# Kernel optimization log

Measured on AMD Instinct MI355X. Metric: run time of the kernel, lower is better.

Reference implementation:

```python
import jax, jax.numpy as jnp
import numpy as np

COUNT = 8  # hardcoded 8x8 patch grid in the original module


def setup_inputs() -> dict:
    key = jax.random.key(0)
    kx, = jax.random.split(key, 1)
    x = jax.random.normal(kx, (8, 64, 512, 512), dtype=jnp.float32)
    gamma = jnp.zeros((1,), dtype=jnp.float32)  # nn.Parameter(torch.zeros(1))
    return {"x": x, "gamma": gamma}


def reference(x, gamma):
    B, C, H, W = x.shape
    s = H // COUNT  # stride; original uses height-derived stride for both dims
    # Extract the 8x8 grid of patches without loops:
    # (B,C,H,W) -> (B,C,cnt,s,cnt,s) -> (B,cnt,cnt,C,s,s) -> (B,P,C,s*s)
    p = x.reshape(B, C, COUNT, s, COUNT, s)
    p = p.transpose(0, 2, 4, 1, 3, 5).reshape(B, COUNT * COUNT, C, s * s)
    # channel-channel energy per patch: [B,P,C,C]
    energy = jnp.einsum('bpci,bpdi->bpcd', p, p)
    # DANet trick: max - energy, then softmax over last dim
    energy_new = jnp.max(energy, axis=-1, keepdims=True) - energy
    attention = jax.nn.softmax(energy_new, axis=-1)
    out = jnp.einsum('bpcd,bpdi->bpci', attention, p)
    # reassemble spatial map
    out = out.reshape(B, COUNT, COUNT, C, s, s)
    out = out.transpose(0, 3, 1, 4, 2, 5).reshape(B, C, H, W)
    # NOTE: in the torch code y = x is an alias and x is overwritten in-place,
    # so the final result is gamma * attended + attended.
    return gamma[0] * out + out
```

## Files before the change

kernel.cpp:

```cpp
#include <hip/hip_runtime.h>


#define NW  512
#define HWs 262144
#define NS1 16
#define NS3 16

typedef __attribute__((ext_vector_type(8)))  __bf16 bf8;
typedef __attribute__((ext_vector_type(4)))  __bf16 bf4;
typedef __attribute__((ext_vector_type(16))) float  f32x16;

#define F4C(v, k) ((k) == 0 ? (v).x : (k) == 1 ? (v).y : (k) == 2 ? (v).z : (v).w)

__device__ __forceinline__ void bar_lgkm() {
  asm volatile("s_waitcnt lgkmcnt(0)" ::: "memory");
  __builtin_amdgcn_s_barrier();
}

__device__ __forceinline__ void load1(const float* g1, int st, float4 (&R)[16]) {
  const float* gp = g1 + (size_t)st * 4 * NW;
#pragma unroll
  for (int rl = 0; rl < 4; ++rl)
#pragma unroll
    for (int j = 0; j < 4; ++j)
      R[rl * 4 + j] = *(const float4*)(gp + (size_t)rl * NW + j * 4);
}

__device__ __forceinline__ void cvtw1(char* wH, char* wL, int q_ld, int swzw,
                                      const float4 (&R)[16]) {
#pragma unroll
  for (int rl = 0; rl < 4; ++rl)
#pragma unroll
    for (int s = 0; s < 2; ++s) {
      const float4 va = R[rl * 4 + s * 2], vb = R[rl * 4 + s * 2 + 1];
      const float f[8] = {va.x, va.y, va.z, va.w, vb.x, vb.y, vb.z, vb.w};
      bf8 h, lo;
#pragma unroll
      for (int e = 0; e < 8; ++e) {
        h[e]  = (__bf16)f[e];
        lo[e] = (__bf16)(f[e] - (float)h[e]);
      }
      const int boff = (rl * 128 + q_ld * 32 + s * 16) ^ swzw;
      *(bf8*)(wH + boff) = h;
      *(bf8*)(wL + boff) = lo;
    }
}

__device__ __forceinline__ void load3(const float* g3, int st, float4 (&R)[16]) {
  const float* gp = g3 + (size_t)st * 4 * NW;
#pragma unroll
  for (int cc = 0; cc < 4; ++cc)
#pragma unroll
    for (int j = 0; j < 4; ++j)
      R[cc * 4 + j] = *(const float4*)(gp + (size_t)cc * HWs + j * 4);
}

__device__ __forceinline__ void cvtw3(char* sT, int cg, int iq, const float4 (&R)[16]) {
#pragma unroll
  for (int w = 0; w < 16; ++w) {
    bf4 q;
#pragma unroll
    for (int cc = 0; cc < 4; ++cc)
      q[cc] = (__bf16)F4C(R[cc * 4 + (w >> 2)], w & 3);
    const int iloc = iq * 16 + w;
    const int sw   = ((iloc & 15) ^ ((iloc >> 4) & 7)) << 4;
    const int boff = (iloc & 127) * 256 + ((((iloc >> 7) << 7) + cg * 8) ^ sw);
    *(bf4*)(sT + boff) = q;
  }
}

extern "C" __global__ __launch_bounds__(256, 2)
void spectralAgg_kernel(const float* __restrict__ x, const float* __restrict__ g,
                        float* __restrict__ out) {
  __shared__ char lds[73728];
  char* sH = lds;
  char* sL = lds + 32768;
  char* sA = lds + 65536;

  const int t   = threadIdx.x;
  const int wv  = t >> 6;
  const int l   = t & 63;
  const int l31 = l & 31;
  const int hh  = l >> 5;

  const int wg = blockIdx.x;
  const int b  = wg >> 6;
  const int pp = wg & 63;
  const int pr = pp >> 3, pc = pp & 7;
  const size_t pbase = (size_t)b * 64 * HWs + (size_t)(pr * 64) * NW + (size_t)(pc * 64);
  const float* xp = x + pbase;
  float* op = out + pbase;

  const int c_ld = t >> 2, q_ld = t & 3;
  const float* g1 = xp + (size_t)c_ld * HWs + q_ld * 16;
  char* wH = sH + c_ld * 512;
  char* wL = sL + c_ld * 512;
  const int swzw = (c_ld & 31) << 4;

  const int ct = wv >> 1, dt = wv & 1;
  const char* pA  = sH + (size_t)(ct * 32 + l31) * 512;
  const char* pBh = sH + (size_t)(dt * 32 + l31) * 512;
  const char* pBl = sL + (size_t)(dt * 32 + l31) * 512;
  const int swzr = l31 << 4;

  f32x16 accG, accS;
#pragma unroll
  for (int r = 0; r < 16; ++r) { accG[r] = 0.f; accS[r] = 0.f; }

  float4 ra[16], rb[16];
  load1(g1, 0, ra);

  for (int st = 0; st < NS1; ++st) {
    load1(g1, (st + 1 < NS1) ? st + 1 : st, rb);
    cvtw1(wH, wL, q_ld, swzw, ra);
    bar_lgkm();
#pragma unroll
    for (int k0 = 0; k0 < 16; ++k0) {
      const int off = (k0 * 32 + hh * 16) ^ swzr;
      const bf8 a  = *(const bf8*)(pA  + off);
      const bf8 bh = *(const bf8*)(pBh + off);
      const bf8 bl = *(const bf8*)(pBl + off);
      accG = __builtin_amdgcn_mfma_f32_32x32x16_bf16(a, bh, accG, 0, 0, 0);
      accS = __builtin_amdgcn_mfma_f32_32x32x16_bf16(a, bl, accS, 0, 0, 0);
    }
    bar_lgkm();
#pragma unroll
    for (int e = 0; e < 16; ++e) ra[e] = rb[e];
  }

  float* S_lds = (float*)sL;
  float* E_lds = (float*)sH;
#pragma unroll
  for (int r = 0; r < 16; ++r) {
    const int cr = ct * 32 + (r & 3) + ((r >> 2) << 3) + (hh << 2);
    S_lds[cr * 64 + dt * 32 + l31] = accS[r];
  }
  bar_lgkm();
#pragma unroll
  for (int r = 0; r < 16; ++r) {
    const int cr = ct * 32 + (r & 3) + ((r >> 2) << 3) + (hh << 2);
    const int d  = dt * 32 + l31;
    E_lds[cr * 64 + d] = accG[r] + accS[r] + S_lds[d * 64 + cr];
  }
  bar_lgkm();

  const int cg = t >> 4, iq = t & 15;
  const float* g3 = xp + (size_t)(cg * 4) * HWs + (size_t)(iq >> 2) * NW + (iq & 3) * 16;
  load3(g3, 0, ra);

  const float gs = 1.0f + g[0];
#pragma unroll 1
  for (int rr = 0; rr < 16; ++rr) {
    const int c = wv * 16 + rr;
    const float e = E_lds[c * 64 + l];
    float mn = e;
#pragma unroll
    for (int o = 32; o; o >>= 1) mn = fminf(mn, __shfl_xor(mn, o));
    const float w = __expf(mn - e);
    float s = w;
#pragma unroll
    for (int o = 32; o; o >>= 1) s += __shfl_xor(s, o);
    const float a = gs * w / s;
    *(__bf16*)(sA + c * 128 + ((l * 2) ^ ((c & 7) << 4))) = (__bf16)a;
  }
  bar_lgkm();

  bf8 bfr[2][4];
#pragma unroll
  for (int c2 = 0; c2 < 2; ++c2)
#pragma unroll
    for (int k0 = 0; k0 < 4; ++k0)
      bfr[c2][k0] = *(const bf8*)(sA + (size_t)(c2 * 32 + l31) * 128 +
                                  ((k0 * 32 + hh * 16) ^ ((l31 & 7) << 4)));

  for (int st = 0; st < NS3; ++st) {
    load3(g3, (st + 1 < NS3) ? st + 1 : st, rb);
    cvtw3(sH, cg, iq, ra);
    bar_lgkm();

    f32x16 oo[2][2];
#pragma unroll
    for (int it = 0; it < 2; ++it)
#pragma unroll
      for (int c2 = 0; c2 < 2; ++c2)
#pragma unroll
        for (int r = 0; r < 16; ++r) oo[it][c2][r] = 0.f;

#pragma unroll
    for (int it = 0; it < 2; ++it) {
      const int i = wv * 64 + it * 32 + l31;
      const char* base = sH + (size_t)(i & 127) * 256;
      const int hb = (i >> 7) * 128;
      const int sw = ((i & 15) ^ ((i >> 4) & 7)) << 4;
#pragma unroll
      for (int k0 = 0; k0 < 4; ++k0) {
        const bf8 pa = *(const bf8*)(base + ((hb + k0 * 32 + hh * 16) ^ sw));
        oo[it][0] = __builtin_amdgcn_mfma_f32_32x32x16_bf16(pa, bfr[0][k0], oo[it][0], 0, 0, 0);
        oo[it][1] = __builtin_amdgcn_mfma_f32_32x32x16_bf16(pa, bfr[1][k0], oo[it][1], 0, 0, 0);
      }
    }

#pragma unroll
    for (int it = 0; it < 2; ++it)
#pragma unroll
      for (int c2 = 0; c2 < 2; ++c2) {
        const size_t cof = (size_t)(c2 * 32 + l31) * HWs;
#pragma unroll
        for (int rq = 0; rq < 4; ++rq) {
          const int iloc = wv * 64 + it * 32 + rq * 8 + hh * 4;
          const int grow = st * 4 + (iloc >> 6), gcol = iloc & 63;
          float4 q;
          q.x = oo[it][c2][rq * 4 + 0];
          q.y = oo[it][c2][rq * 4 + 1];
          q.z = oo[it][c2][rq * 4 + 2];
          q.w = oo[it][c2][rq * 4 + 3];
          *(float4*)(op + cof + (size_t)grow * NW + gcol) = q;
        }
      }
    bar_lgkm();
#pragma unroll
    for (int e = 0; e < 16; ++e) ra[e] = rb[e];
  }
}

extern "C" void kernel_launch(void* const* d_in, const int* in_sizes, int n_in,
                              void* d_out, int out_size, void* d_ws, size_t ws_size,
                              hipStream_t stream) {
  const float* x = (const float*)d_in[0];
  const float* g = (const float*)d_in[1];
  float* o = (float*)d_out;
  spectralAgg_kernel<<<dim3(512), dim3(256), 0, stream>>>(x, g, o);
}
```

Before: 378.0 us.

## Double block to 512 threads with split-K Gram and halved register staging

Raises the workgroup to 512 threads (8 waves). The Gram phase now splits the K dimension across two wave halves and reduces their partial results through LDS, and each thread stages fewer fp32 loads (8 float4 instead of 32). The second phase re-lays out the transposed patch tile with a padded 144-byte row stride, and LDS shrinks to 64KB so more waves can be resident. The aim is more latency hiding and less register pressure, at the cost of extra LDS reduction passes and barriers.

New measurement: 387.9 us. 2.6% more time.

```diff
diff --git a/kernel.cpp b/kernel.cpp
--- a/kernel.cpp
+++ b/kernel.cpp
@@ -1,122 +1,82 @@
 #include <hip/hip_runtime.h>
 
 
-#define NW  512
-#define HWs 262144
-#define NS1 16
-#define NS3 16
+#define NW   512
+#define HWs  262144
+#define NS   16
 
 typedef __attribute__((ext_vector_type(8)))  __bf16 bf8;
 typedef __attribute__((ext_vector_type(4)))  __bf16 bf4;
 typedef __attribute__((ext_vector_type(16))) float  f32x16;
 
-#define F4C(v, k) ((k) == 0 ? (v).x : (k) == 1 ? (v).y : (k) == 2 ? (v).z : (v).w)
+#define F4E(v,j) ((j)==0?(v).x:(j)==1?(v).y:(j)==2?(v).z:(v).w)
 
 __device__ __forceinline__ void bar_lgkm() {
   asm volatile("s_waitcnt lgkmcnt(0)" ::: "memory");
   __builtin_amdgcn_s_barrier();
 }
 
-__device__ __forceinline__ void load1(const float* g1, int st, float4 (&R)[16]) {
-  const float* gp = g1 + (size_t)st * 4 * NW;
-#pragma unroll
-  for (int rl = 0; rl < 4; ++rl)
-#pragma unroll
-    for (int j = 0; j < 4; ++j)
-      R[rl * 4 + j] = *(const float4*)(gp + (size_t)rl * NW + j * 4);
-}
-
-__device__ __forceinline__ void cvtw1(char* wH, char* wL, int q_ld, int swzw,
-                                      const float4 (&R)[16]) {
-#pragma unroll
-  for (int rl = 0; rl < 4; ++rl)
-#pragma unroll
-    for (int s = 0; s < 2; ++s) {
-      const float4 va = R[rl * 4 + s * 2], vb = R[rl * 4 + s * 2 + 1];
-      const float f[8] = {va.x, va.y, va.z, va.w, vb.x, vb.y, vb.z, vb.w};
-      bf8 h, lo;
-#pragma unroll
-      for (int e = 0; e < 8; ++e) {
-        h[e]  = (__bf16)f[e];
-        lo[e] = (__bf16)(f[e] - (float)h[e]);
-      }
-      const int boff = (rl * 128 + q_ld * 32 + s * 16) ^ swzw;
-      *(bf8*)(wH + boff) = h;
-      *(bf8*)(wL + boff) = lo;
-    }
-}
-
-__device__ __forceinline__ void load3(const float* g3, int st, float4 (&R)[16]) {
-  const float* gp = g3 + (size_t)st * 4 * NW;
-#pragma unroll
-  for (int cc = 0; cc < 4; ++cc)
-#pragma unroll
-    for (int j = 0; j < 4; ++j)
-      R[cc * 4 + j] = *(const float4*)(gp + (size_t)cc * HWs + j * 4);
-}
-
-__device__ __forceinline__ void cvtw3(char* sT, int cg, int iq, const float4 (&R)[16]) {
-#pragma unroll
-  for (int w = 0; w < 16; ++w) {
-    bf4 q;
-#pragma unroll
-    for (int cc = 0; cc < 4; ++cc)
-      q[cc] = (__bf16)F4C(R[cc * 4 + (w >> 2)], w & 3);
-    const int iloc = iq * 16 + w;
-    const int sw   = ((iloc & 15) ^ ((iloc >> 4) & 7)) << 4;
-    const int boff = (iloc & 127) * 256 + ((((iloc >> 7) << 7) + cg * 8) ^ sw);
-    *(bf4*)(sT + boff) = q;
-  }
-}
-
-extern "C" __global__ __launch_bounds__(256, 2)
+extern "C" __global__ __launch_bounds__(512, 4)
 void spectralAgg_kernel(const float* __restrict__ x, const float* __restrict__ g,
                         float* __restrict__ out) {
-  __shared__ char lds[73728];
+  __shared__ char lds[65536];
   char* sH = lds;
   char* sL = lds + 32768;
-  char* sA = lds + 65536;
-
-  const int t   = threadIdx.x;
-  const int wv  = t >> 6;
-  const int l   = t & 63;
+  char* sA = lds + 49152;
+
+  const int T   = threadIdx.x;
+  const int wv8 = T >> 6;
+  const int l   = T & 63;
   const int l31 = l & 31;
   const int hh  = l >> 5;
+  const int g2  = (T >> 4) & 3;
+  const int e16 = T & 15;
 
   const int wg = blockIdx.x;
   const int b  = wg >> 6;
   const int pp = wg & 63;
-  const int pr = pp >> 3, pc = pp & 7;
-  const size_t pbase = (size_t)b * 64 * HWs + (size_t)(pr * 64) * NW + (size_t)(pc * 64);
+  const size_t pbase = (size_t)b*64*HWs + (size_t)((pp>>3)*64)*NW + (size_t)((pp&7)*64);
   const float* xp = x + pbase;
   float* op = out + pbase;
 
-  const int c_ld = t >> 2, q_ld = t & 3;
-  const float* g1 = xp + (size_t)c_ld * HWs + q_ld * 16;
-  char* wH = sH + c_ld * 512;
-  char* wL = sL + c_ld * 512;
-  const int swzw = (c_ld & 31) << 4;
-
-  const int ct = wv >> 1, dt = wv & 1;
-  const char* pA  = sH + (size_t)(ct * 32 + l31) * 512;
-  const char* pBh = sH + (size_t)(dt * 32 + l31) * 512;
-  const char* pBl = sL + (size_t)(dt * 32 + l31) * 512;
-  const int swzr = l31 << 4;
+  float4 ra[8];
+#pragma unroll
+  for (int k = 0; k < 8; ++k)
+    ra[k] = *(const float4*)(xp + (size_t)(k*8+wv8)*HWs + (size_t)g2*NW + e16*4);
+
+  const int q  = wv8 & 3;
+  const int kh = wv8 >> 2;
+  const int ct = q >> 1, dt = q & 1;
+  const char* pA  = sH + (size_t)(ct*32+l31)*512 + kh*256;
+  const char* pBh = sH + (size_t)(dt*32+l31)*512 + kh*256;
+  const char* pBl = sL + (size_t)(dt*32+l31)*512 + kh*256;
+  const int swz1 = (l31 & 15) << 4;
 
   f32x16 accG, accS;
 #pragma unroll
   for (int r = 0; r < 16; ++r) { accG[r] = 0.f; accS[r] = 0.f; }
 
-  float4 ra[16], rb[16];
-  load1(g1, 0, ra);
-
-  for (int st = 0; st < NS1; ++st) {
-    load1(g1, (st + 1 < NS1) ? st + 1 : st, rb);
-    cvtw1(wH, wL, q_ld, swzw, ra);
-    bar_lgkm();
-#pragma unroll
-    for (int k0 = 0; k0 < 16; ++k0) {
-      const int off = (k0 * 32 + hh * 16) ^ swzr;
+  for (int st = 0; st < NS; ++st) {
+#pragma unroll
+    for (int k = 0; k < 8; ++k) {
+      const int c = k*8 + wv8;
+      const float4 v = ra[k];
+      bf4 h, lo;
+      h[0]=(__bf16)v.x; h[1]=(__bf16)v.y; h[2]=(__bf16)v.z; h[3]=(__bf16)v.w;
+      lo[0]=(__bf16)(v.x-(float)h[0]); lo[1]=(__bf16)(v.y-(float)h[1]);
+      lo[2]=(__bf16)(v.z-(float)h[2]); lo[3]=(__bf16)(v.w-(float)h[3]);
+      const int off = c*512 + ((g2*128 + e16*8) ^ ((c&15)<<4));
+      *(bf4*)(sH+off) = h;
+      *(bf4*)(sL+off) = lo;
+    }
+    const int sn = (st+1 < NS) ? st+1 : st;
+#pragma unroll
+    for (int k = 0; k < 8; ++k)
+      ra[k] = *(const float4*)(xp + (size_t)(k*8+wv8)*HWs + (size_t)(sn*4+g2)*NW + e16*4);
+    bar_lgkm();
+#pragma unroll
+    for (int k0 = 0; k0 < 8; ++k0) {
+      const int off = (k0*32 + hh*16) ^ swz1;
       const bf8 a  = *(const bf8*)(pA  + off);
       const bf8 bh = *(const bf8*)(pBh + off);
       const bf8 bl = *(const bf8*)(pBl + off);
@@ -124,35 +84,50 @@
       accS = __builtin_amdgcn_mfma_f32_32x32x16_bf16(a, bl, accS, 0, 0, 0);
     }
     bar_lgkm();
-#pragma unroll
-    for (int e = 0; e < 16; ++e) ra[e] = rb[e];
-  }
-
+  }
+
+  float* E_lds = (float*)sH;
   float* S_lds = (float*)sL;
-  float* E_lds = (float*)sH;
-#pragma unroll
-  for (int r = 0; r < 16; ++r) {
-    const int cr = ct * 32 + (r & 3) + ((r >> 2) << 3) + (hh << 2);
-    S_lds[cr * 64 + dt * 32 + l31] = accS[r];
-  }
-  bar_lgkm();
-#pragma unroll
-  for (int r = 0; r < 16; ++r) {
-    const int cr = ct * 32 + (r & 3) + ((r >> 2) << 3) + (hh << 2);
-    const int d  = dt * 32 + l31;
-    E_lds[cr * 64 + d] = accG[r] + accS[r] + S_lds[d * 64 + cr];
-  }
-  bar_lgkm();
-
-  const int cg = t >> 4, iq = t & 15;
-  const float* g3 = xp + (size_t)(cg * 4) * HWs + (size_t)(iq >> 2) * NW + (iq & 3) * 16;
-  load3(g3, 0, ra);
+  if (kh == 0) {
+#pragma unroll
+    for (int r = 0; r < 16; ++r) {
+      const int cr = ct*32 + (r&3) + ((r>>2)<<3) + (hh<<2);
+      const int d  = dt*32 + l31;
+      S_lds[cr*64+d] = accS[r];
+      E_lds[cr*64+d] = accG[r] + accS[r];
+    }
+  }
+  bar_lgkm();
+  if (kh == 1) {
+#pragma unroll
+    for (int r = 0; r < 16; ++r) {
+      const int cr = ct*32 + (r&3) + ((r>>2)<<3) + (hh<<2);
+      const int d  = dt*32 + l31;
+      S_lds[cr*64+d] += accS[r];
+      E_lds[cr*64+d] += accG[r] + accS[r];
+    }
+  }
+  bar_lgkm();
+#pragma unroll
+  for (int r = 0; r < 8; ++r) {
+    const int c = T >> 3, d = (T&7)*8 + r;
+    E_lds[c*64+d] += S_lds[d*64+c];
+  }
+  bar_lgkm();
+
+  const int quad = (wv8*4+g2) & 15;
+  const int rwb  = (wv8*4+g2) >> 4;
+#pragma unroll
+  for (int k = 0; k < 8; ++k) {
+    const int cc = k & 3, mm = k >> 2;
+    ra[k] = *(const float4*)(xp + (size_t)(quad*4+cc)*HWs + (size_t)(rwb+mm*2)*NW + e16*4);
+  }
 
   const float gs = 1.0f + g[0];
 #pragma unroll 1
-  for (int rr = 0; rr < 16; ++rr) {
-    const int c = wv * 16 + rr;
-    const float e = E_lds[c * 64 + l];
+  for (int rr = 0; rr < 8; ++rr) {
+    const int c = wv8*8 + rr;
+    const float e = E_lds[c*64 + l];
     float mn = e;
 #pragma unroll
     for (int o = 32; o; o >>= 1) mn = fminf(mn, __shfl_xor(mn, o));
@@ -161,65 +136,63 @@
 #pragma unroll
     for (int o = 32; o; o >>= 1) s += __shfl_xor(s, o);
     const float a = gs * w / s;
-    *(__bf16*)(sA + c * 128 + ((l * 2) ^ ((c & 7) << 4))) = (__bf16)a;
-  }
-  bar_lgkm();
-
-  bf8 bfr[2][4];
-#pragma unroll
-  for (int c2 = 0; c2 < 2; ++c2)
-#pragma unroll
-    for (int k0 = 0; k0 < 4; ++k0)
-      bfr[c2][k0] = *(const bf8*)(sA + (size_t)(c2 * 32 + l31) * 128 +
-                                  ((k0 * 32 + hh * 16) ^ ((l31 & 7) << 4)));
-
-  for (int st = 0; st < NS3; ++st) {
-    load3(g3, (st + 1 < NS3) ? st + 1 : st, rb);
-    cvtw3(sH, cg, iq, ra);
-    bar_lgkm();
-
-    f32x16 oo[2][2];
-#pragma unroll
-    for (int it = 0; it < 2; ++it)
-#pragma unroll
-      for (int c2 = 0; c2 < 2; ++c2)
-#pragma unroll
-        for (int r = 0; r < 16; ++r) oo[it][c2][r] = 0.f;
-
-#pragma unroll
-    for (int it = 0; it < 2; ++it) {
-      const int i = wv * 64 + it * 32 + l31;
-      const char* base = sH + (size_t)(i & 127) * 256;
-      const int hb = (i >> 7) * 128;
-      const int sw = ((i & 15) ^ ((i >> 4) & 7)) << 4;
-#pragma unroll
-      for (int k0 = 0; k0 < 4; ++k0) {
-        const bf8 pa = *(const bf8*)(base + ((hb + k0 * 32 + hh * 16) ^ sw));
-        oo[it][0] = __builtin_amdgcn_mfma_f32_32x32x16_bf16(pa, bfr[0][k0], oo[it][0], 0, 0, 0);
-        oo[it][1] = __builtin_amdgcn_mfma_f32_32x32x16_bf16(pa, bfr[1][k0], oo[it][1], 0, 0, 0);
+    *(__bf16*)(sA + c*256 + ((l*2) ^ ((c&15)<<4))) = (__bf16)a;
+  }
+  bar_lgkm();
+
+  char* sT = sH;
+  const char* pP = sT + (size_t)(wv8*32 + l31)*144;
+
+  for (int st = 0; st < NS; ++st) {
+#pragma unroll
+    for (int mm = 0; mm < 2; ++mm) {
+      const int row = rwb + mm*2;
+#pragma unroll
+      for (int jj = 0; jj < 4; ++jj) {
+        const int i = row*64 + e16*4 + jj;
+        bf4 qv;
+        qv[0] = (__bf16)F4E(ra[mm*4+0], jj);
+        qv[1] = (__bf16)F4E(ra[mm*4+1], jj);
+        qv[2] = (__bf16)F4E(ra[mm*4+2], jj);
+        qv[3] = (__bf16)F4E(ra[mm*4+3], jj);
+        *(bf4*)(sT + i*144 + quad*8) = qv;
       }
     }
-
-#pragma unroll
-    for (int it = 0; it < 2; ++it)
-#pragma unroll
-      for (int c2 = 0; c2 < 2; ++c2) {
-        const size_t cof = (size_t)(c2 * 32 + l31) * HWs;
-#pragma unroll
-        for (int rq = 0; rq < 4; ++rq) {
-          const int iloc = wv * 64 + it * 32 + rq * 8 + hh * 4;
-          const int grow = st * 4 + (iloc >> 6), gcol = iloc & 63;
-          float4 q;
-          q.x = oo[it][c2][rq * 4 + 0];
-          q.y = oo[it][c2][rq * 4 + 1];
-          q.z = oo[it][c2][rq * 4 + 2];
-          q.w = oo[it][c2][rq * 4 + 3];
-          *(float4*)(op + cof + (size_t)grow * NW + gcol) = q;
-        }
-      }
-    bar_lgkm();
-#pragma unroll
-    for (int e = 0; e < 16; ++e) ra[e] = rb[e];
+    const int sn = (st+1 < NS) ? st+1 : st;
+#pragma unroll
+    for (int k = 0; k < 8; ++k) {
+      const int cc = k & 3, mm = k >> 2;
+      ra[k] = *(const float4*)(xp + (size_t)(quad*4+cc)*HWs + (size_t)(sn*4+rwb+mm*2)*NW + e16*4);
+    }
+    bar_lgkm();
+
+    f32x16 oo0, oo1;
+#pragma unroll
+    for (int r = 0; r < 16; ++r) { oo0[r] = 0.f; oo1[r] = 0.f; }
+#pragma unroll
+    for (int k0 = 0; k0 < 4; ++k0) {
+      const int sAoff = (k0*32 + hh*16) ^ ((l31&15)<<4);
+      const bf8 pa = *(const bf8*)(pP + k0*32 + hh*16);
+      const bf8 b0 = *(const bf8*)(sA + (size_t)l31*256 + sAoff);
+      const bf8 b1 = *(const bf8*)(sA + (size_t)(32+l31)*256 + sAoff);
+      oo0 = __builtin_amdgcn_mfma_f32_32x32x16_bf16(pa, b0, oo0, 0, 0, 0);
+      oo1 = __builtin_amdgcn_mfma_f32_32x32x16_bf16(pa, b1, oo1, 0, 0, 0);
+    }
+
+#pragma unroll
+    for (int rq = 0; rq < 4; ++rq) {
+      const int iloc = wv8*32 + rq*8 + hh*4;
+      const int gi = st*256 + iloc;
+      const int grow = gi >> 6, gcol = gi & 63;
+      float* oprow = op + (size_t)grow*NW + gcol;
+      float4 q0; q0.x = oo0[rq*4+0]; q0.y = oo0[rq*4+1];
+                 q0.z = oo0[rq*4+2]; q0.w = oo0[rq*4+3];
+      *(float4*)(oprow + (size_t)l31*HWs) = q0;
+      float4 q1; q1.x = oo1[rq*4+0]; q1.y = oo1[rq*4+1];
+                 q1.z = oo1[rq*4+2]; q1.w = oo1[rq*4+3];
+      *(float4*)(oprow + (size_t)(32+l31)*HWs) = q1;
+    }
+    bar_lgkm();
   }
 }
 
@@ -229,5 +202,5 @@
   const float* x = (const float*)d_in[0];
   const float* g = (const float*)d_in[1];
   float* o = (float*)d_out;
-  spectralAgg_kernel<<<dim3(512), dim3(256), 0, stream>>>(x, g, o);
+  spectralAgg_kernel<<<dim3(512), dim3(512), 0, stream>>>(x, g, o);
 }
```

## Split into gram, softmax, and PV kernels with row-strip coalesced loads

Applied to the files above, without the earlier changes.

Replaces the single per-patch kernel with three kernels. In the first and third, each block covers a 16-row strip across all eight patches of a patch row, so global loads and stores run along full 512-wide rows instead of 64-wide patch segments. The first kernel writes partial Gram matrices to workspace, a small kernel sums them and applies the softmax, and the third kernel transposes x in LDS before doing the attention-times-values MFMA. This costs a second read of x, extra workspace traffic and two more launches, and it falls back to the old kernel when the workspace is too small.

New measurement: 412.5 us. 1.09x slower.

```diff
diff --git a/kernel.cpp b/kernel.cpp
--- a/kernel.cpp
+++ b/kernel.cpp
@@ -3,21 +3,245 @@
 
 #define NW  512
 #define HWs 262144
-#define NS1 16
-#define NS3 16
-
+
+typedef __attribute__((ext_vector_type(4)))  __bf16 bf4;
 typedef __attribute__((ext_vector_type(8)))  __bf16 bf8;
-typedef __attribute__((ext_vector_type(4)))  __bf16 bf4;
 typedef __attribute__((ext_vector_type(16))) float  f32x16;
 
-#define F4C(v, k) ((k) == 0 ? (v).x : (k) == 1 ? (v).y : (k) == 2 ? (v).z : (v).w)
+#define MFMA __builtin_amdgcn_mfma_f32_32x32x16_bf16
+#define F4E(v,j) ((j)==0?(v).x:(j)==1?(v).y:(j)==2?(v).z:(v).w)
 
 __device__ __forceinline__ void bar_lgkm() {
   asm volatile("s_waitcnt lgkmcnt(0)" ::: "memory");
   __builtin_amdgcn_s_barrier();
 }
 
-__device__ __forceinline__ void load1(const float* g1, int st, float4 (&R)[16]) {
+__device__ __forceinline__ int soff(int c, int rb) {
+  return c * 1024 + (rb & 512) + ((rb & 511) ^ ((c & 31) << 4));
+}
+
+extern "C" __global__ __launch_bounds__(512, 2)
+void k1_gram(const float* __restrict__ x, float* __restrict__ ep) {
+  __shared__ char lds[133120];
+  char* sHi = lds;
+  char* sLo = lds + 65536;
+  float* S_lds = (float*)lds;
+
+  const int t   = threadIdx.x;
+  const int w8  = t >> 6;
+  const int l   = t & 63;
+  const int l31 = l & 31, hh = l >> 5;
+  const int pc  = w8;
+  const int cld = t >> 7;
+  const int hf  = (t >> 6) & 1;
+
+  const int bid = blockIdx.x;
+  const int b  = bid >> 5;
+  const int pr = (bid >> 2) & 7;
+  const int hq = bid & 3;
+  const float* xb = x + (size_t)b * 64 * HWs + (size_t)(pr * 64 + hq * 16) * NW
+                  + hf * 256 + l * 4;
+
+  f32x16 aG00, aG01, aG10, aG11, aS00, aS01, aS10, aS11;
+#pragma unroll
+  for (int i = 0; i < 16; ++i) {
+    aG00[i]=0.f; aG01[i]=0.f; aG10[i]=0.f; aG11[i]=0.f;
+    aS00[i]=0.f; aS01[i]=0.f; aS10[i]=0.f; aS11[i]=0.f;
+  }
+
+  float4 ra[16];
+#pragma unroll
+  for (int j = 0; j < 16; ++j)
+    ra[j] = *(const float4*)(xb + (size_t)(j * 4 + cld) * HWs);
+
+  for (int r = 0; r < 16; ++r) {
+#pragma unroll
+    for (int j = 0; j < 16; ++j) {
+      const int c = j * 4 + cld;
+      const float4 v = ra[j];
+      bf4 h, lo;
+      h[0]=(__bf16)v.x; h[1]=(__bf16)v.y; h[2]=(__bf16)v.z; h[3]=(__bf16)v.w;
+      lo[0]=(__bf16)(v.x-(float)h[0]); lo[1]=(__bf16)(v.y-(float)h[1]);
+      lo[2]=(__bf16)(v.z-(float)h[2]); lo[3]=(__bf16)(v.w-(float)h[3]);
+      const int wb = c * 1024 + hf * 512 + ((l * 8) ^ ((c & 31) << 4));
+      *(bf4*)(sHi + wb) = h;
+      *(bf4*)(sLo + wb) = lo;
+    }
+    if (r + 1 < 16) {
+#pragma unroll
+      for (int j = 0; j < 16; ++j)
+        ra[j] = *(const float4*)(xb + (size_t)(j * 4 + cld) * HWs
+                                 + (size_t)(r + 1) * NW);
+    }
+    bar_lgkm();
+#pragma unroll
+    for (int ks = 0; ks < 4; ++ks) {
+      const int rb = pc * 128 + ks * 32 + hh * 16;
+      const bf8 a0 = *(const bf8*)(sHi + soff(l31, rb));
+      const bf8 a1 = *(const bf8*)(sHi + soff(32 + l31, rb));
+      const bf8 q0 = *(const bf8*)(sLo + soff(l31, rb));
+      const bf8 q1 = *(const bf8*)(sLo + soff(32 + l31, rb));
+      aG00 = MFMA(a0, a0, aG00, 0, 0, 0);
+      aG01 = MFMA(a0, a1, aG01, 0, 0, 0);
+      aG10 = MFMA(a1, a0, aG10, 0, 0, 0);
+      aG11 = MFMA(a1, a1, aG11, 0, 0, 0);
+      aS00 = MFMA(a0, q0, aS00, 0, 0, 0);
+      aS01 = MFMA(a0, q1, aS01, 0, 0, 0);
+      aS10 = MFMA(a1, q0, aS10, 0, 0, 0);
+      aS11 = MFMA(a1, q1, aS11, 0, 0, 0);
+    }
+    bar_lgkm();
+  }
+
+#pragma unroll
+  for (int i = 0; i < 16; ++i) {
+    const int rr = (i & 3) + ((i >> 2) << 3) + (hh << 2);
+    S_lds[pc * 4160 + (rr)      * 65 + l31]      = aS00[i];
+    S_lds[pc * 4160 + (rr)      * 65 + 32 + l31] = aS01[i];
+    S_lds[pc * 4160 + (32 + rr) * 65 + l31]      = aS10[i];
+    S_lds[pc * 4160 + (32 + rr) * 65 + 32 + l31] = aS11[i];
+  }
+  bar_lgkm();
+  const int pat = b * 64 + pr * 8 + pc;
+  float* epb = ep + ((size_t)(pat * 4 + hq) << 12);
+#pragma unroll
+  for (int i = 0; i < 16; ++i) {
+    const int rr = (i & 3) + ((i >> 2) << 3) + (hh << 2);
+    epb[(rr)      * 64 + l31]      = aG00[i] + aS00[i] + S_lds[pc*4160 + (l31)    *65 + rr];
+    epb[(rr)      * 64 + 32 + l31] = aG01[i] + aS01[i] + S_lds[pc*4160 + (32+l31) *65 + rr];
+    epb[(32 + rr) * 64 + l31]      = aG10[i] + aS10[i] + S_lds[pc*4160 + (l31)    *65 + 32 + rr];
+    epb[(32 + rr) * 64 + 32 + l31] = aG11[i] + aS11[i] + S_lds[pc*4160 + (32+l31) *65 + 32 + rr];
+  }
+}
+
+extern "C" __global__ __launch_bounds__(256)
+void k2_softmax(const float* __restrict__ ep, const float* __restrict__ g,
+                __bf16* __restrict__ attn) {
+  const int pat = blockIdx.x;
+  const int w4 = threadIdx.x >> 6, l = threadIdx.x & 63;
+  const float gs = 1.0f + g[0];
+  const float* e0 = ep + ((size_t)(pat * 4) << 12);
+#pragma unroll 1
+  for (int cc = 0; cc < 16; ++cc) {
+    const int c = w4 * 16 + cc;
+    const int o = c * 64 + l;
+    const float e = e0[o] + e0[4096 + o] + e0[8192 + o] + e0[12288 + o];
+    float mn = e;
+#pragma unroll
+    for (int off = 32; off; off >>= 1) mn = fminf(mn, __shfl_xor(mn, off));
+    const float w = __expf(mn - e);
+    float s = w;
+#pragma unroll
+    for (int off = 32; off; off >>= 1) s += __shfl_xor(s, off);
+    attn[(size_t)pat * 4096 + o] = (__bf16)(gs * w / s);
+  }
+}
+
+extern "C" __global__ __launch_bounds__(512, 2)
+void k3_pv(const float* __restrict__ x, const __bf16* __restrict__ attn,
+           float* __restrict__ out) {
+  __shared__ char lds[139264];
+  char* nat = lds;
+  char* pT  = lds + 65536;
+
+  const int t   = threadIdx.x;
+  const int w8  = t >> 6;
+  const int l   = t & 63;
+  const int l31 = l & 31, hh = l >> 5;
+  const int pc  = w8;
+  const int cld = t >> 7;
+  const int hf  = (t >> 6) & 1;
+  const int cb  = t & 15;
+  const int wb0 = t >> 4;
+
+  const int bid = blockIdx.x;
+  const int b  = bid >> 5;
+  const int pr = (bid >> 2) & 7;
+  const int hq = bid & 3;
+  const float* xb = x + (size_t)b * 64 * HWs + (size_t)(pr * 64 + hq * 16) * NW
+                  + hf * 256 + l * 4;
+  float* ob = out + (size_t)b * 64 * HWs + (size_t)(pr * 64 + hq * 16) * NW;
+  const int pat = b * 64 + pr * 8 + pc;
+
+  bf8 af0[4], af1[4];
+#pragma unroll
+  for (int ks = 0; ks < 4; ++ks) {
+    af0[ks] = *(const bf8*)(attn + (size_t)pat * 4096 + (l31)      * 64 + ks * 16 + hh * 8);
+    af1[ks] = *(const bf8*)(attn + (size_t)pat * 4096 + (32 + l31) * 64 + ks * 16 + hh * 8);
+  }
+
+  float4 ra[16];
+#pragma unroll
+  for (int j = 0; j < 16; ++j)
+    ra[j] = *(const float4*)(xb + (size_t)(j * 4 + cld) * HWs);
+
+  for (int r = 0; r < 16; ++r) {
+#pragma unroll
+    for (int j = 0; j < 16; ++j) {
+      const int c = j * 4 + cld;
+      const float4 v = ra[j];
+      bf4 h;
+      h[0]=(__bf16)v.x; h[1]=(__bf16)v.y; h[2]=(__bf16)v.z; h[3]=(__bf16)v.w;
+      *(bf4*)(nat + c * 1024 + hf * 512 + ((l * 8) ^ ((c & 31) << 4))) = h;
+    }
+    if (r + 1 < 16) {
+#pragma unroll
+      for (int j = 0; j < 16; ++j)
+        ra[j] = *(const float4*)(xb + (size_t)(j * 4 + cld) * HWs
+                                 + (size_t)(r + 1) * NW);
+    }
+    bar_lgkm();
+#pragma unroll
+    for (int kk = 0; kk < 4; ++kk) {
+      const int w0 = (wb0 + kk * 32) * 4;
+      bf4 rd0, rd1, rd2, rd3;
+      {
+        const int c0 = cb * 4;
+        const int hfb = (w0 >> 8) * 512;
+        const int ib2 = (w0 & 255) * 2;
+        rd0 = *(const bf4*)(nat + (c0    ) * 1024 + hfb + (ib2 ^ (((c0    ) & 31) << 4)));
+        rd1 = *(const bf4*)(nat + (c0 + 1) * 1024 + hfb + (ib2 ^ (((c0 + 1) & 31) << 4)));
+        rd2 = *(const bf4*)(nat + (c0 + 2) * 1024 + hfb + (ib2 ^ (((c0 + 2) & 31) << 4)));
+        rd3 = *(const bf4*)(nat + (c0 + 3) * 1024 + hfb + (ib2 ^ (((c0 + 3) & 31) << 4)));
+      }
+#pragma unroll
+      for (int jj = 0; jj < 4; ++jj) {
+        bf4 wv;
+        wv[0] = rd0[jj]; wv[1] = rd1[jj]; wv[2] = rd2[jj]; wv[3] = rd3[jj];
+        *(bf4*)(pT + (size_t)(w0 + jj) * 144 + cb * 8) = wv;
+      }
+    }
+    bar_lgkm();
+#pragma unroll
+    for (int ib = 0; ib < 2; ++ib) {
+      f32x16 o0, o1;
+#pragma unroll
+      for (int i = 0; i < 16; ++i) { o0[i] = 0.f; o1[i] = 0.f; }
+      const char* prow = pT + (size_t)(pc * 64 + ib * 32 + l31) * 144;
+#pragma unroll
+      for (int ks = 0; ks < 4; ++ks) {
+        const bf8 pa = *(const bf8*)(prow + ks * 32 + hh * 16);
+        o0 = MFMA(pa, af0[ks], o0, 0, 0, 0);
+        o1 = MFMA(pa, af1[ks], o1, 0, 0, 0);
+      }
+#pragma unroll
+      for (int rq = 0; rq < 4; ++rq) {
+        const int wloc = pc * 64 + ib * 32 + rq * 8 + hh * 4;
+        float* orow = ob + (size_t)r * NW + wloc;
+        float4 q0; q0.x=o0[rq*4+0]; q0.y=o0[rq*4+1]; q0.z=o0[rq*4+2]; q0.w=o0[rq*4+3];
+        *(float4*)(orow + (size_t)l31 * HWs) = q0;
+        float4 q1; q1.x=o1[rq*4+0]; q1.y=o1[rq*4+1]; q1.z=o1[rq*4+2]; q1.w=o1[rq*4+3];
+        *(float4*)(orow + (size_t)(32 + l31) * HWs) = q1;
+      }
+    }
+    bar_lgkm();
+  }
+}
+
+#define NS1 16
+#define NS3 16
+
+__device__ __forceinline__ void fb_load1(const float* g1, int st, float4 (&R)[16]) {
   const float* gp = g1 + (size_t)st * 4 * NW;
 #pragma unroll
   for (int rl = 0; rl < 4; ++rl)
@@ -25,9 +249,8 @@
     for (int j = 0; j < 4; ++j)
       R[rl * 4 + j] = *(const float4*)(gp + (size_t)rl * NW + j * 4);
 }
-
-__device__ __forceinline__ void cvtw1(char* wH, char* wL, int q_ld, int swzw,
-                                      const float4 (&R)[16]) {
+__device__ __forceinline__ void fb_cvtw1(char* wH, char* wL, int q_ld, int swzw,
+                                         const float4 (&R)[16]) {
 #pragma unroll
   for (int rl = 0; rl < 4; ++rl)
 #pragma unroll
@@ -36,17 +259,13 @@
       const float f[8] = {va.x, va.y, va.z, va.w, vb.x, vb.y, vb.z, vb.w};
       bf8 h, lo;
 #pragma unroll
-      for (int e = 0; e < 8; ++e) {
-        h[e]  = (__bf16)f[e];
-        lo[e] = (__bf16)(f[e] - (float)h[e]);
-      }
+      for (int e = 0; e < 8; ++e) { h[e] = (__bf16)f[e]; lo[e] = (__bf16)(f[e] - (float)h[e]); }
       const int boff = (rl * 128 + q_ld * 32 + s * 16) ^ swzw;
       *(bf8*)(wH + boff) = h;
       *(bf8*)(wL + boff) = lo;
     }
 }
-
-__device__ __forceinline__ void load3(const float* g3, int st, float4 (&R)[16]) {
+__device__ __forceinline__ void fb_load3(const float* g3, int st, float4 (&R)[16]) {
   const float* gp = g3 + (size_t)st * 4 * NW;
 #pragma unroll
   for (int cc = 0; cc < 4; ++cc)
@@ -54,105 +273,85 @@
     for (int j = 0; j < 4; ++j)
       R[cc * 4 + j] = *(const float4*)(gp + (size_t)cc * HWs + j * 4);
 }
-
-__device__ __forceinline__ void cvtw3(char* sT, int cg, int iq, const float4 (&R)[16]) {
+__device__ __forceinline__ void fb_cvtw3(char* sT, int cg, int iq, const float4 (&R)[16]) {
 #pragma unroll
   for (int w = 0; w < 16; ++w) {
     bf4 q;
 #pragma unroll
-    for (int cc = 0; cc < 4; ++cc)
-      q[cc] = (__bf16)F4C(R[cc * 4 + (w >> 2)], w & 3);
+    for (int cc = 0; cc < 4; ++cc) q[cc] = (__bf16)F4E(R[cc * 4 + (w >> 2)], w & 3);
     const int iloc = iq * 16 + w;
-    const int sw   = ((iloc & 15) ^ ((iloc >> 4) & 7)) << 4;
+    const int sw = ((iloc & 15) ^ ((iloc >> 4) & 7)) << 4;
     const int boff = (iloc & 127) * 256 + ((((iloc >> 7) << 7) + cg * 8) ^ sw);
     *(bf4*)(sT + boff) = q;
   }
 }
-
 extern "C" __global__ __launch_bounds__(256, 2)
-void spectralAgg_kernel(const float* __restrict__ x, const float* __restrict__ g,
-                        float* __restrict__ out) {
+void spectralAgg_fallback(const float* __restrict__ x, const float* __restrict__ g,
+                          float* __restrict__ out) {
   __shared__ char lds[73728];
   char* sH = lds;
   char* sL = lds + 32768;
   char* sA = lds + 65536;
-
-  const int t   = threadIdx.x;
-  const int wv  = t >> 6;
-  const int l   = t & 63;
-  const int l31 = l & 31;
-  const int hh  = l >> 5;
-
-  const int wg = blockIdx.x;
-  const int b  = wg >> 6;
-  const int pp = wg & 63;
-  const int pr = pp >> 3, pc = pp & 7;
-  const size_t pbase = (size_t)b * 64 * HWs + (size_t)(pr * 64) * NW + (size_t)(pc * 64);
+  const int t = threadIdx.x, wv = t >> 6, l = t & 63, l31 = l & 31, hh = l >> 5;
+  const int wg = blockIdx.x, b = wg >> 6, pp = wg & 63, pr = pp >> 3, pcq = pp & 7;
+  const size_t pbase = (size_t)b*64*HWs + (size_t)(pr*64)*NW + (size_t)(pcq*64);
   const float* xp = x + pbase;
   float* op = out + pbase;
-
   const int c_ld = t >> 2, q_ld = t & 3;
   const float* g1 = xp + (size_t)c_ld * HWs + q_ld * 16;
   char* wH = sH + c_ld * 512;
   char* wL = sL + c_ld * 512;
   const int swzw = (c_ld & 31) << 4;
-
   const int ct = wv >> 1, dt = wv & 1;
-  const char* pA  = sH + (size_t)(ct * 32 + l31) * 512;
-  const char* pBh = sH + (size_t)(dt * 32 + l31) * 512;
-  const char* pBl = sL + (size_t)(dt * 32 + l31) * 512;
+  const char* pA  = sH + (size_t)(ct*32+l31)*512;
+  const char* pBh = sH + (size_t)(dt*32+l31)*512;
+  const char* pBl = sL + (size_t)(dt*32+l31)*512;
   const int swzr = l31 << 4;
-
   f32x16 accG, accS;
 #pragma unroll
-  for (int r = 0; r < 16; ++r) { accG[r] = 0.f; accS[r] = 0.f; }
-
+  for (int i = 0; i < 16; ++i) { accG[i] = 0.f; accS[i] = 0.f; }
   float4 ra[16], rb[16];
-  load1(g1, 0, ra);
-
+  fb_load1(g1, 0, ra);
   for (int st = 0; st < NS1; ++st) {
-    load1(g1, (st + 1 < NS1) ? st + 1 : st, rb);
-    cvtw1(wH, wL, q_ld, swzw, ra);
+    fb_load1(g1, (st + 1 < NS1) ? st + 1 : st, rb);
+    fb_cvtw1(wH, wL, q_ld, swzw, ra);
     bar_lgkm();
 #pragma unroll
     for (int k0 = 0; k0 < 16; ++k0) {
       const int off = (k0 * 32 + hh * 16) ^ swzr;
-      const bf8 a  = *(const bf8*)(pA  + off);
+      const bf8 a  = *(const bf8*)(pA + off);
       const bf8 bh = *(const bf8*)(pBh + off);
       const bf8 bl = *(const bf8*)(pBl + off);
-      accG = __builtin_amdgcn_mfma_f32_32x32x16_bf16(a, bh, accG, 0, 0, 0);
-      accS = __builtin_amdgcn_mfma_f32_32x32x16_bf16(a, bl, accS, 0, 0, 0);
+      accG = MFMA(a, bh, accG, 0, 0, 0);
+      accS = MFMA(a, bl, accS, 0, 0, 0);
     }
     bar_lgkm();
 #pragma unroll
     for (int e = 0; e < 16; ++e) ra[e] = rb[e];
   }
-
   float* S_lds = (float*)sL;
   float* E_lds = (float*)sH;
 #pragma unroll
-  for (int r = 0; r < 16; ++r) {
-    const int cr = ct * 32 + (r & 3) + ((r >> 2) << 3) + (hh << 2);
-    S_lds[cr * 64 + dt * 32 + l31] = accS[r];
+  for (int i = 0; i < 16; ++i) {
+    const int cr = ct*32 + (i&3) + ((i>>2)<<3) + (hh<<2);
+    S_lds[cr*64 + dt*32 + l31] = accS[i];
   }
   bar_lgkm();
 #pragma unroll
-  for (int r = 0; r < 16; ++r) {
-    const int cr = ct * 32 + (r & 3) + ((r >> 2) << 3) + (hh << 2);
-    const int d  = dt * 32 + l31;
-    E_lds[cr * 64 + d] = accG[r] + accS[r] + S_lds[d * 64 + cr];
+  for (int i = 0; i < 16; ++i) {
+    const int cr = ct*32 + (i&3) + ((i>>2)<<3) + (hh<<2);
+    const int d = dt*32 + l31;
+    E_lds[cr*64 + d] = accG[i] + accS[i] + S_lds[d*64 + cr];
   }
   bar_lgkm();
-
   const int cg = t >> 4, iq = t & 15;
-  const float* g3 = xp + (size_t)(cg * 4) * HWs + (size_t)(iq >> 2) * NW + (iq & 3) * 16;
-  load3(g3, 0, ra);
-
+  const float* g3 = xp + (size_t)(cg*4)*HWs + (size_t)(iq>>2)*NW + (iq&3)*16;
+  fb_load3(g3, 0, ra);
   const float gs = 1.0f + g[0];
 #pragma unroll 1
   for (int rr = 0; rr < 16; ++rr) {
-    const int c = wv * 16 + rr;
-    const float e = E_lds[c * 64 + l];
+    const int c = wv*16 + rr;
+    const float e = E_lds[c*64 + l];
     float mn = e;
 #pragma unroll
     for (int o = 32; o; o >>= 1) mn = fminf(mn, __shfl_xor(mn, o));
@@ -160,62 +359,49 @@
     float s = w;
 #pragma unroll
     for (int o = 32; o; o >>= 1) s += __shfl_xor(s, o);
-    const float a = gs * w / s;
-    *(__bf16*)(sA + c * 128 + ((l * 2) ^ ((c & 7) << 4))) = (__bf16)a;
+    *(__bf16*)(sA + c*128 + ((l*2) ^ ((c&7)<<4))) = (__bf16)(gs * w / s);
   }
   bar_lgkm();
-
   bf8 bfr[2][4];
 #pragma unroll
   for (int c2 = 0; c2 < 2; ++c2)
 #pragma unroll
     for (int k0 = 0; k0 < 4; ++k0)
-      bfr[c2][k0] = *(const bf8*)(sA + (size_t)(c2 * 32 + l31) * 128 +
-                                  ((k0 * 32 + hh * 16) ^ ((l31 & 7) << 4)));
-
+      bfr[c2][k0] = *(const bf8*)(sA + (size_t)(c2*32+l31)*128 +
+                                  ((k0*32 + hh*16) ^ ((l31&7)<<4)));
   for (int st = 0; st < NS3; ++st) {
-    load3(g3, (st + 1 < NS3) ? st + 1 : st, rb);
-    cvtw3(sH, cg, iq, ra);
-    bar_lgkm();
-
-    f32x16 oo[2][2];
+    fb_load3(g3, (st + 1 < NS3) ? st + 1 : st, rb);
+    fb_cvtw3(sH, cg, iq, ra);
+    bar_lgkm();
+    f32x16 oo0[2], oo1[2];
 #pragma unroll
     for (int it = 0; it < 2; ++it)
 #pragma unroll
-      for (int c2 = 0; c2 < 2; ++c2)
-#pragma unroll
-        for (int r = 0; r < 16; ++r) oo[it][c2][r] = 0.f;
-
+      for (int i = 0; i < 16; ++i) { oo0[it][i] = 0.f; oo1[it][i] = 0.f; }
 #pragma unroll
     for (int it = 0; it < 2; ++it) {
-      const int i = wv * 64 + it * 32 + l31;
+      const int i = wv*64 + it*32 + l31;
       const char* base = sH + (size_t)(i & 127) * 256;
       const int hb = (i >> 7) * 128;
       const int sw = ((i & 15) ^ ((i >> 4) & 7)) << 4;
 #pragma unroll
       for (int k0 = 0; k0 < 4; ++k0) {
-        const bf8 pa = *(const bf8*)(base + ((hb + k0 * 32 + hh * 16) ^ sw));
-        oo[it][0] = __builtin_amdgcn_mfma_f32_32x32x16_bf16(pa, bfr[0][k0], oo[it][0], 0, 0, 0);
-        oo[it][1] = __builtin_amdgcn_mfma_f32_32x32x16_bf16(pa, bfr[1][k0], oo[it][1], 0, 0, 0);
-      }
-    }
-
+        const bf8 pa = *(const bf8*)(base + ((hb + k0*32 + hh*16) ^ sw));
+        oo0[it] = MFMA(pa, bfr[0][k0], oo0[it], 0, 0, 0);
+        oo1[it] = MFMA(pa, bfr[1][k0], oo1[it], 0, 0, 0);
+      }
+    }
 #pragma unroll
     for (int it = 0; it < 2; ++it)
 #pragma unroll
-      for (int c2 = 0; c2 < 2; ++c2) {
-        const size_t cof = (size_t)(c2 * 32 + l31) * HWs;
-#pragma unroll
-        for (int rq = 0; rq < 4; ++rq) {
-          const int iloc = wv * 64 + it * 32 + rq * 8 + hh * 4;
-          const int grow = st * 4 + (iloc >> 6), gcol = iloc & 63;
-          float4 q;
-          q.x = oo[it][c2][rq * 4 + 0];
-          q.y = oo[it][c2][rq * 4 + 1];
-          q.z = oo[it][c2][rq * 4 + 2];
-          q.w = oo[it][c2][rq * 4 + 3];
-          *(float4*)(op + cof + (size_t)grow * NW + gcol) = q;
-        }
+      for (int rq = 0; rq < 4; ++rq) {
+        const int iloc = wv*64 + it*32 + rq*8 + hh*4;
+        const int gi = st*256 + iloc;
+        float* oprow = op + (size_t)(gi >> 6)*NW + (gi & 63);
+        float4 q0; q0.x=oo0[it][rq*4+0]; q0.y=oo0[it][rq*4+1]; q0.z=oo0[it][rq*4+2]; q0.w=oo0[it][rq*4+3];
+        *(float4*)(oprow + (size_t)l31*HWs) = q0;
+        float4 q1; q1.x=oo1[it][rq*4+0]; q1.y=oo1[it][rq*4+1]; q1.z=oo1[it][rq*4+2]; q1.w=oo1[it][rq*4+3];
+        *(float4*)(oprow + (size_t)(32+l31)*HWs) = q1;
       }
     bar_lgkm();
 #pragma unroll
@@ -229,5 +415,14 @@
   const float* x = (const float*)d_in[0];
   const float* g = (const float*)d_in[1];
   float* o = (float*)d_out;
-  spectralAgg_kernel<<<dim3(512), dim3(256), 0, stream>>>(x, g, o);
-}
+  const size_t need = (size_t)512 * 4 * 4096 * 4 + (size_t)512 * 4096 * 2;
+  if (ws_size >= need) {
+    float* ep = (float*)d_ws;
+    __bf16* attn = (__bf16*)((char*)d_ws + (size_t)512 * 4 * 4096 * 4);
+    k1_gram<<<dim3(256), dim3(512), 0, stream>>>(x, ep);
+    k2_softmax<<<dim3(512), dim3(256), 0, stream>>>(ep, g, attn);
+    k3_pv<<<dim3(256), dim3(512), 0, stream>>>(x, attn, o);
+  } else {
+    spectralAgg_fallback<<<dim3(512), dim3(256), 0, stream>>>(x, g, o);
+  }
+}
```
